# Performance work log

Measured on AMD Instinct MI355X. Metric: run time of the kernel, lower is better.

## Reference

```python
import jax, jax.numpy as jnp
import numpy as np
import math

H = 128      # hidden_channels
R = 32       # num_rbf
N = 4096     # atoms
E = 65536    # edges
CU = 4.5     # cutoff_upper (cutoff_lower = 0)
ALPHA = 5.0 / CU
MEANS = jnp.linspace(math.exp(-CU), 1.0, R, dtype=jnp.float32)
BETA = jnp.float32((2.0 / R * (1.0 - math.exp(-CU))) ** -2)
EPS = 1e-5


def _ln(x, g, b):
    mu = x.mean(-1, keepdims=True)
    var = ((x - mu) ** 2).mean(-1, keepdims=True)
    return (x - mu) * jax.lax.rsqrt(var + EPS) * g + b


def setup_inputs() -> dict:
    key = jax.random.key(0)
    ks = jax.random.split(key, 20)
    f32 = jnp.float32

    def w(i, shape):
        return jax.random.normal(ks[i], shape, f32) / np.float32(np.sqrt(shape[-1]))

    return {
        "edge_vec": jax.random.normal(ks[0], (E, 3), f32) * 1.5,
        "emb_w": w(1, (128, H)),
        "emb2_w": w(2, (H, 2 * H)), "emb2_b": jnp.zeros((H,), f32),
        "dp1_w": w(3, (H, R)), "dp1_b": jnp.zeros((H,), f32),
        "dp2_w": w(4, (H, R)), "dp2_b": jnp.zeros((H,), f32),
        "dp3_w": w(5, (H, R)), "dp3_b": jnp.zeros((H,), f32),
        "lt0_w": w(6, (H, H)), "lt1_w": w(7, (H, H)), "lt2_w": w(8, (H, H)),
        "ls0_w": w(9, (2 * H, H)), "ls0_b": jnp.zeros((2 * H,), f32),
        "ls1_w": w(10, (3 * H, 2 * H)), "ls1_b": jnp.zeros((3 * H,), f32),
        "init_g": jnp.ones((H,), f32), "init_b": jnp.zeros((H,), f32),
        "lin_w": w(11, (H, 3 * H)), "lin_b": jnp.zeros((H,), f32),
        "outn_g": jnp.ones((3 * H,), f32), "outn_b": jnp.zeros((3 * H,), f32),
        "ol1_w": w(12, (H // 2, H)), "ol1_b": jnp.zeros((H // 2,), f32),
        "ol2_w": w(13, (1, H // 2)), "ol2_b": jnp.zeros((1,), f32),
        "z": jax.random.randint(ks[14], (N,), 0, 128, dtype=jnp.int32),
        "edge_index": jax.random.randint(ks[15], (2, E), 0, N, dtype=jnp.int32),
    }


def reference(edge_vec, emb_w, emb2_w, emb2_b, dp1_w, dp1_b, dp2_w, dp2_b,
              dp3_w, dp3_b, lt0_w, lt1_w, lt2_w, ls0_w, ls0_b, ls1_w, ls1_b,
              init_g, init_b, lin_w, lin_b, outn_g, outn_b, ol1_w, ol1_b,
              ol2_w, ol2_b, z, edge_index):
    n = z.shape[0]
    src, dst = edge_index[0], edge_index[1]

    d = jnp.sqrt((edge_vec ** 2).sum(-1))                 # (E,)
    vn = edge_vec / d[:, None]                             # unit edge vectors
    cut = jnp.where(d < CU, 0.5 * (jnp.cos(jnp.pi * d / CU) + 1.0), 0.0)
    # expnorm RBF
    rbf = cut[:, None] * jnp.exp(-BETA * (jnp.exp(-ALPHA * d)[:, None] - MEANS) ** 2)  # (E,R)

    # atomic-number message Zij = emb2(cat(emb(z_i), emb(z_j)))
    zpair = jnp.concatenate([emb_w[z[src]], emb_w[z[dst]]], -1)  # (E,2H)
    zij = zpair @ emb2_w.T + emb2_b                              # (E,H)
    c = cut[:, None] * zij                                       # cutoff * Zij, (E,H)

    w1 = (rbf @ dp1_w.T + dp1_b) * c    # scalar channel weights (E,H)
    w2 = (rbf @ dp2_w.T + dp2_b) * c
    w3 = (rbf @ dp3_w.T + dp3_b) * c

    eye = jnp.eye(3, dtype=edge_vec.dtype)
    zero = jnp.zeros_like(vn[:, 0])
    skew = jnp.stack([zero, -vn[:, 2], vn[:, 1],
                      vn[:, 2], zero, -vn[:, 0],
                      -vn[:, 1], vn[:, 0], zero], 1).reshape(-1, 3, 3)  # (E,3,3)
    outer = vn[:, :, None] * vn[:, None, :]
    sym = outer - ((vn ** 2).sum(-1) / 3.0)[:, None, None] * eye        # traceless sym (E,3,3)

    seg = lambda a: jax.ops.segment_sum(a, src, num_segments=n)
    I0 = seg(w1)[:, :, None, None] * eye                                # (N,H,3,3)
    A0 = seg(w2[:, :, None, None] * skew[:, None, :, :])                # (N,H,3,3)
    S0 = seg(w3[:, :, None, None] * sym[:, None, :, :])                 # (N,H,3,3)

    tn = ((I0 + A0 + S0) ** 2).sum((-2, -1))                            # tensor_norm, (N,H)
    nrm = _ln(tn, init_g, init_b)
    h = jax.nn.silu(nrm @ ls0_w.T + ls0_b)
    scal = jax.nn.silu(h @ ls1_w.T + ls1_b).reshape(n, H, 3)            # per-channel gates

    I1 = jnp.einsum('nhxy,gh->ngxy', I0, lt0_w) * scal[..., 0][..., None, None]
    A1 = jnp.einsum('nhxy,gh->ngxy', A0, lt1_w) * scal[..., 1][..., None, None]
    S1 = jnp.einsum('nhxy,gh->ngxy', S0, lt2_w) * scal[..., 2][..., None, None]

    x = jnp.concatenate([(I1 ** 2).sum((-2, -1)),
                         (A1 ** 2).sum((-2, -1)),
                         (S1 ** 2).sum((-2, -1))], -1)                  # (N,3H)
    x = _ln(x, outn_g, outn_b)
    s1 = x @ lin_w.T + lin_b
    s2 = jax.nn.silu(s1) @ ol1_w.T + ol1_b
    s3 = jax.nn.silu(s2) @ ol2_w.T + ol2_b                              # per-atom energy (N,1)
    return s3
```

## Files before the change

kernel.cpp:

```cpp
#include <hip/hip_runtime.h>
#include <math.h>

#define NH_TOT 524288
#define N_ATOM 4096
#define N_EDGE 65536

typedef __attribute__((ext_vector_type(8))) short bf16x8;
typedef __attribute__((ext_vector_type(4))) float f32x4;

__device__ __forceinline__ unsigned short f2bf(float f) {
    unsigned u = __builtin_bit_cast(unsigned, f);
    unsigned r = (u + 0x7fffu + ((u >> 16) & 1u)) >> 16;
    return (unsigned short)r;
}
__device__ __forceinline__ float silu(float v) { return v / (1.0f + expf(-v)); }

#define WB_LS1 32768
#define WB_LT0 131072
#define WB_LT1 147456
#define WB_LT2 163840
#define WB_DP  180224

__global__ __launch_bounds__(256) void k_setup(
    const float* __restrict__ emb_w, const float* __restrict__ emb2_w,
    const int* __restrict__ ei,
    const float* __restrict__ ls0_w, const float* __restrict__ ls1_w,
    const float* __restrict__ lt0_w, const float* __restrict__ lt1_w,
    const float* __restrict__ lt2_w,
    const float* __restrict__ dp1_w, const float* __restrict__ dp2_w,
    const float* __restrict__ dp3_w,
    float* __restrict__ U1, float* __restrict__ U2,
    int* __restrict__ cnt, unsigned short* __restrict__ wb) {
    const int bx = blockIdx.x, tid = threadIdx.x;
    if (bx < 64) {
        __shared__ float se[2][128];
        const int t = bx * 2 + (tid >> 7), h = tid & 127, half = tid >> 7;
        se[half][h] = emb_w[t * 128 + h];
        __syncthreads();
        float u1 = 0.f, u2 = 0.f;
        const float* row = emb2_w + h * 256;
#pragma unroll 8
        for (int k = 0; k < 128; k++) {
            u1 += se[half][k] * row[k];
            u2 += se[half][k] * row[128 + k];
        }
        U1[t * 128 + h] = u1;
        U2[t * 128 + h] = u2;
    } else if (bx < 320) {
        const int e = (bx - 64) * 256 + tid;
        atomicAdd(&cnt[ei[e]], 1);
    } else {
        const int base = (bx - 320) * 1024 + tid * 4;
        const float* src;
        int off;
        if (base < 32768)       { src = ls0_w; off = 0; }
        else if (base < 131072) { src = ls1_w; off = 32768; }
        else if (base < 147456) { src = lt0_w; off = 131072; }
        else if (base < 163840) { src = lt1_w; off = 147456; }
        else if (base < 180224) { src = lt2_w; off = 163840; }
        else if (base < 184320) { src = dp1_w; off = 180224; }
        else if (base < 188416) { src = dp2_w; off = 184320; }
        else                    { src = dp3_w; off = 188416; }
        const float4 v = *(const float4*)(src + (base - off));
        unsigned short* o = wb + base;
        o[0] = f2bf(v.x); o[1] = f2bf(v.y); o[2] = f2bf(v.z); o[3] = f2bf(v.w);
    }
}

__global__ __launch_bounds__(256) void k_scan(const int* __restrict__ cnt, int* __restrict__ off) {
    __shared__ int s[256];
    const int t = threadIdx.x;
    int loc[16];
    int run = 0;
#pragma unroll
    for (int i = 0; i < 16; i++) { run += cnt[t * 16 + i]; loc[i] = run; }
    s[t] = run;
    __syncthreads();
    for (int d = 1; d < 256; d <<= 1) {
        const int add = (t >= d) ? s[t - d] : 0;
        __syncthreads();
        s[t] += add;
        __syncthreads();
    }
    const int base = s[t] - run;
    if (t == 0) off[0] = 0;
#pragma unroll
    for (int i = 0; i < 16; i++) off[t * 16 + i + 1] = base + loc[i];
}

__global__ __launch_bounds__(256) void k_edge(
    const float* __restrict__ edge_vec, const int* __restrict__ ei,
    const int* __restrict__ z, const int* __restrict__ off,
    int* __restrict__ cursor,
    unsigned short* __restrict__ rbf_bf, float4* __restrict__ geom,
    int* __restrict__ u2off) {
    const int e = blockIdx.x * 256 + threadIdx.x;
    const int src = ei[e];
    const int pos = off[src] + atomicAdd(&cursor[src], 1);

    const float evx = edge_vec[3 * e + 0];
    const float evy = edge_vec[3 * e + 1];
    const float evz = edge_vec[3 * e + 2];
    const float d = sqrtf(evx * evx + evy * evy + evz * evz);
    const float inv = 1.0f / d;
    const float cut = (d < 4.5f) ? 0.5f * (cosf(0.6981317007977318f * d) + 1.0f) : 0.0f;
    geom[pos] = make_float4(evx * inv, evy * inv, evz * inv, cut);
    u2off[pos] = z[ei[N_EDGE + e]] << 7;

    const float expd = expf(-1.1111111111111112f * d);
    const float m0 = 0.011108996538242306f;
    const float dm = (1.0f - m0) * (1.0f / 31.0f);
    const float tb = 0.0625f * (1.0f - m0);
    const float beta = 1.0f / (tb * tb);
    unsigned int rb[16];
#pragma unroll
    for (int r = 0; r < 16; r++) {
        const float df0 = expd - (m0 + (float)(2 * r) * dm);
        const float df1 = expd - (m0 + (float)(2 * r + 1) * dm);
        const unsigned lo = f2bf(cut * expf(-beta * df0 * df0));
        const unsigned hi = f2bf(cut * expf(-beta * df1 * df1));
        rb[r] = lo | (hi << 16);
    }
    uint4* dst = (uint4*)(rbf_bf + (size_t)pos * 32);
#pragma unroll
    for (int j = 0; j < 4; j++)
        dst[j] = make_uint4(rb[4 * j], rb[4 * j + 1], rb[4 * j + 2], rb[4 * j + 3]);
}

__global__ __launch_bounds__(256) void k_node(
    const int* __restrict__ z, const int* __restrict__ off,
    const unsigned short* __restrict__ rbf_bf, const float4* __restrict__ geom,
    const int* __restrict__ u2off,
    const float* __restrict__ U1, const float* __restrict__ U2,
    const float* __restrict__ emb2_b,
    const float* __restrict__ dp1_b, const float* __restrict__ dp2_b,
    const float* __restrict__ dp3_b,
    const unsigned short* __restrict__ wb,
    const float* __restrict__ init_g, const float* __restrict__ init_b,
    unsigned short* __restrict__ acc_bf, unsigned short* __restrict__ nrm_bf) {
    const int n = blockIdx.x, tid = threadIdx.x;
    const int wave = tid >> 6, lane = tid & 63, lm = lane & 15, lq = lane >> 4;
    const int beg = off[n];
    const int En = off[n + 1] - beg;
    const int zoff = z[n] << 7;

    const unsigned short* dpw = wb + WB_DP;
    bf16x8 bfr[3][2];
    float u1c[2], bhc[2], bk1[2], bk2[2], bk3[2];
    int cols[2];
#pragma unroll
    for (int t = 0; t < 2; t++) {
        const int col = wave * 32 + t * 16 + lm;
        cols[t] = col;
        u1c[t] = U1[zoff + col];
        bhc[t] = emb2_b[col];
        bk1[t] = dp1_b[col]; bk2[t] = dp2_b[col]; bk3[t] = dp3_b[col];
#pragma unroll
        for (int k = 0; k < 3; k++)
            bfr[k][t] = *(const bf16x8*)(dpw + k * 4096 + col * 32 + lq * 8);
    }

    float part[10][2];
#pragma unroll
    for (int p = 0; p < 10; p++) { part[p][0] = 0.f; part[p][1] = 0.f; }

    for (int mi = 0; mi < En; mi += 16) {
        const int arow = beg + min(mi + lm, En - 1);
        const bf16x8 af = *(const bf16x8*)(rbf_bf + (size_t)arow * 32 + lq * 8);
        f32x4 c[3][2];
#pragma unroll
        for (int k = 0; k < 3; k++)
#pragma unroll
            for (int t = 0; t < 2; t++)
                c[k][t] = __builtin_amdgcn_mfma_f32_16x16x32_bf16(
                    af, bfr[k][t], (f32x4){0.f, 0.f, 0.f, 0.f}, 0, 0, 0);
#pragma unroll
        for (int r = 0; r < 4; r++) {
            const int er = mi + lq * 4 + r;
            const bool valid = er < En;
            const int p = beg + (valid ? er : 0);
            const float4 g = geom[p];
            const int u2o = u2off[p];
#pragma unroll
            for (int t = 0; t < 2; t++) {
                const float u2v = U2[u2o + cols[t]];
                const float cc = valid ? g.w * (u1c[t] + u2v + bhc[t]) : 0.f;
                const float w1 = (c[0][t][r] + bk1[t]) * cc;
                const float w2 = (c[1][t][r] + bk2[t]) * cc;
                const float w3 = (c[2][t][r] + bk3[t]) * cc;
                part[0][t] += w1;
                part[1][t] += w2 * g.x; part[2][t] += w2 * g.y; part[3][t] += w2 * g.z;
                const float tx = w3 * g.x, ty = w3 * g.y;
                part[4][t] += tx * g.x; part[5][t] += tx * g.y; part[6][t] += tx * g.z;
                part[7][t] += ty * g.y; part[8][t] += ty * g.z; part[9][t] += w3 * g.z * g.z;
            }
        }
    }

    __shared__ float sP[10][128];
    __shared__ float red[128];

#pragma unroll
    for (int p = 0; p < 10; p++)
#pragma unroll
        for (int t = 0; t < 2; t++) {
            float v = part[p][t];
            v += __shfl_xor(v, 16, 64);
            v += __shfl_xor(v, 32, 64);
            if (lq == 0) {
                sP[p][cols[t]] = v;
                acc_bf[(size_t)p * NH_TOT + n * 128 + cols[t]] = f2bf(v);
            }
        }
    __syncthreads();

    float tn = 0.f, dv = 0.f;
    if (tid < 128) {
        const int h = tid;
        const float aI = sP[0][h];
        const float axv = sP[1][h], ayv = sP[2][h], azv = sP[3][h];
        const float mxx = sP[4][h], mxy = sP[5][h], mxz = sP[6][h];
        const float myy = sP[7][h], myz = sP[8][h], mzz = sP[9][h];
        const float tr3 = (mxx + myy + mzz) * (1.0f / 3.0f);
        const float t00 = aI + mxx - tr3;
        const float t11 = aI + myy - tr3;
        const float t22 = aI + mzz - tr3;
        tn = t00 * t00 + t11 * t11 + t22 * t22 +
             2.0f * (mxy * mxy + azv * azv + mxz * mxz + ayv * ayv + myz * myz + axv * axv);
        red[tid] = tn;
    }
    __syncthreads();
    for (int s = 64; s > 0; s >>= 1) { if (tid < s) red[tid] += red[tid + s]; __syncthreads(); }
    const float mu = red[0] * (1.0f / 128.0f);
    __syncthreads();
    if (tid < 128) { dv = tn - mu; red[tid] = dv * dv; }
    __syncthreads();
    for (int s = 64; s > 0; s >>= 1) { if (tid < s) red[tid] += red[tid + s]; __syncthreads(); }
    const float var = red[0] * (1.0f / 128.0f);
    if (tid < 128)
        nrm_bf[n * 128 + tid] = f2bf(dv * rsqrtf(var + 1e-5f) * init_g[tid] + init_b[tid]);
}

__global__ __launch_bounds__(256) void k_megatail(
    const unsigned short* __restrict__ nrm_bf, const unsigned short* __restrict__ acc_bf,
    const unsigned short* __restrict__ wb,
    const float* __restrict__ ls0_b, const float* __restrict__ ls1_b,
    const float* __restrict__ outn_g, const float* __restrict__ outn_b,
    const float* __restrict__ lin_w, const float* __restrict__ lin_b,
    const float* __restrict__ ol1_w, const float* __restrict__ ol1_b,
    const float* __restrict__ ol2_w, const float* __restrict__ ol2_b,
    float* __restrict__ out) {
    const int tid = threadIdx.x, wave = tid >> 6, lane = tid & 63;
    const int lm = lane & 15, lq = lane >> 4;
    const int n0 = blockIdx.x * 8;

    __shared__ unsigned short h1[16][280];
    __shared__ float scal_s[8][388];
    __shared__ float xs[8][388];
    __shared__ float ss[8][132];

    {
        f32x4 acc[4];
#pragma unroll
        for (int j = 0; j < 4; j++) acc[j] = (f32x4){0.f, 0.f, 0.f, 0.f};
        const int cbase = wave * 64;
#pragma unroll
        for (int kc = 0; kc < 128; kc += 32) {
            const int arow = n0 + min(lm, 7);
            const bf16x8 af = *(const bf16x8*)(nrm_bf + (size_t)arow * 128 + kc + lq * 8);
#pragma unroll
            for (int sn = 0; sn < 4; sn++) {
                const bf16x8 b = *(const bf16x8*)(wb + (size_t)(cbase + sn * 16 + lm) * 128 + kc + lq * 8);
                acc[sn] = __builtin_amdgcn_mfma_f32_16x16x32_bf16(af, b, acc[sn], 0, 0, 0);
            }
        }
#pragma unroll
        for (int sn = 0; sn < 4; sn++) {
            const int col = cbase + sn * 16 + lm;
            const float bv = ls0_b[col];
#pragma unroll
            for (int r = 0; r < 4; r++)
                h1[lq * 4 + r][col] = f2bf(silu(acc[sn][r] + bv));
        }
    }
    __syncthreads();
    {
        f32x4 acc[6];
#pragma unroll
        for (int j = 0; j < 6; j++) acc[j] = (f32x4){0.f, 0.f, 0.f, 0.f};
        const int cbase = wave * 96;
        const unsigned short* ls1p = wb + WB_LS1;
#pragma unroll 2
        for (int kc = 0; kc < 256; kc += 32) {
            const bf16x8 af = *(const bf16x8*)(&h1[lm][kc + lq * 8]);
#pragma unroll
            for (int sn = 0; sn < 6; sn++) {
                const bf16x8 b = *(const bf16x8*)(ls1p + (size_t)(cbase + sn * 16 + lm) * 256 + kc + lq * 8);
                acc[sn] = __builtin_amdgcn_mfma_f32_16x16x32_bf16(af, b, acc[sn], 0, 0, 0);
            }
        }
#pragma unroll
        for (int sn = 0; sn < 6; sn++) {
            const int col = cbase + sn * 16 + lm;
            const float bv = ls1_b[col];
#pragma unroll
            for (int r = 0; r < 4; r++) {
                const int node = lq * 4 + r;
                if (node < 8) scal_s[node][col] = silu(acc[sn][r] + bv);
            }
        }
    }
    __syncthreads();

    f32x4 e0[2], e1[2], e2[2], trv[2];
#pragma unroll
    for (int sn = 0; sn < 2; sn++) {
        e0[sn] = (f32x4){0.f, 0.f, 0.f, 0.f};
        e1[sn] = (f32x4){0.f, 0.f, 0.f, 0.f};
        e2[sn] = (f32x4){0.f, 0.f, 0.f, 0.f};
        trv[sn] = (f32x4){0.f, 0.f, 0.f, 0.f};
    }
#pragma unroll
    for (int p = 0; p < 10; p++) {
        const unsigned short* A = acc_bf + (size_t)p * NH_TOT;
        const unsigned short* B = wb + (p == 0 ? WB_LT0 : (p < 4 ? WB_LT1 : WB_LT2));
        f32x4 c[2];
        c[0] = (f32x4){0.f, 0.f, 0.f, 0.f};
        c[1] = (f32x4){0.f, 0.f, 0.f, 0.f};
#pragma unroll
        for (int kc = 0; kc < 128; kc += 32) {
            const int arow = n0 + min(lm, 7);
            const bf16x8 af = *(const bf16x8*)(A + (size_t)arow * 128 + kc + lq * 8);
#pragma unroll
            for (int sn = 0; sn < 2; sn++) {
                const bf16x8 b = *(const bf16x8*)(B + (size_t)(wave * 32 + sn * 16 + lm) * 128 + kc + lq * 8);
                c[sn] = __builtin_amdgcn_mfma_f32_16x16x32_bf16(af, b, c[sn], 0, 0, 0);
            }
        }
#pragma unroll
        for (int sn = 0; sn < 2; sn++) {
            if (p == 0)      e0[sn] += c[sn] * c[sn];
            else if (p < 4)  e1[sn] += c[sn] * c[sn];
            else if (p == 4 || p == 7 || p == 9) { e2[sn] += c[sn] * c[sn]; trv[sn] += c[sn]; }
            else             e2[sn] += 2.0f * c[sn] * c[sn];
        }
    }

    if (lq < 2) {
#pragma unroll
        for (int sn = 0; sn < 2; sn++) {
            const int g = wave * 32 + sn * 16 + lm;
#pragma unroll
            for (int r = 0; r < 4; r++) {
                const int node = lq * 4 + r;
                const float s0 = scal_s[node][3 * g + 0];
                const float s1 = scal_s[node][3 * g + 1];
                const float s2 = scal_s[node][3 * g + 2];
                const float a0 = 3.0f * e0[sn][r] * s0 * s0;
                const float a1 = 2.0f * e1[sn][r] * s1 * s1;
                const float tr = trv[sn][r];
                const float a2 = (e2[sn][r] - tr * tr * (1.0f / 3.0f)) * s2 * s2;
                xs[node][g] = a0;
                xs[node][128 + g] = a1;
                xs[node][256 + g] = a2;
            }
        }
    }
    __syncthreads();

#pragma unroll
    for (int i = 0; i < 2; i++) {
        const int node = wave * 2 + i;
        float v[6];
        float s = 0.f;
#pragma unroll
        for (int j = 0; j < 6; j++) { v[j] = xs[node][lane + 64 * j]; s += v[j]; }
#pragma unroll
        for (int o = 1; o < 64; o <<= 1) s += __shfl_xor(s, o, 64);
        const float mu = s * (1.0f / 384.0f);
        float q = 0.f;
#pragma unroll
        for (int j = 0; j < 6; j++) { v[j] -= mu; q += v[j] * v[j]; }
#pragma unroll
        for (int o = 1; o < 64; o <<= 1) q += __shfl_xor(q, o, 64);
        const float rs = rsqrtf(q * (1.0f / 384.0f) + 1e-5f);
#pragma unroll
        for (int j = 0; j < 6; j++) {
            const int col = lane + 64 * j;
            xs[node][col] = v[j] * rs * outn_g[col] + outn_b[col];
        }
    }
    __syncthreads();

    {
        const int j = tid & 127, half = tid >> 7;
        float a4[4];
        const float lb = lin_b[j];
#pragma unroll
        for (int i = 0; i < 4; i++) a4[i] = lb;
        const float4* wr = (const float4*)(lin_w + j * 384);
#pragma unroll 2
        for (int k4 = 0; k4 < 96; k4++) {
            const float4 w4 = wr[k4];
#pragma unroll
            for (int i = 0; i < 4; i++) {
                const float4 xv = *(const float4*)&xs[half * 4 + i][k4 * 4];
                a4[i] += w4.x * xv.x + w4.y * xv.y + w4.z * xv.z + w4.w * xv.w;
            }
        }
#pragma unroll
        for (int i = 0; i < 4; i++) ss[half * 4 + i][j] = silu(a4[i]);
    }
    __syncthreads();

    {
        const int o = tid & 63, q = tid >> 6;
        float a2v[2];
        const float ob = ol1_b[o];
        a2v[0] = ob; a2v[1] = ob;
        const float4* o4 = (const float4*)(ol1_w + o * 128);
#pragma unroll 4
        for (int k4 = 0; k4 < 32; k4++) {
            const float4 w4 = o4[k4];
#pragma unroll
            for (int i = 0; i < 2; i++) {
                const float4 sv = *(const float4*)&ss[q * 2 + i][k4 * 4];
                a2v[i] += w4.x * sv.x + w4.y * sv.y + w4.z * sv.z + w4.w * sv.w;
            }
        }
        const float w2 = ol2_w[o];
#pragma unroll
        for (int i = 0; i < 2; i++) {
            float v = silu(a2v[i]) * w2;
            for (int s = 32; s > 0; s >>= 1) v += __shfl_down(v, s, 64);
            if (o == 0) out[n0 + q * 2 + i] = v + ol2_b[0];
        }
    }
}

extern "C" void kernel_launch(void* const* d_in, const int* in_sizes, int n_in,
                              void* d_out, int out_size, void* d_ws, size_t ws_size,
                              hipStream_t stream) {
    (void)in_sizes; (void)n_in; (void)out_size; (void)ws_size;
    const float* edge_vec = (const float*)d_in[0];
    const float* emb_w   = (const float*)d_in[1];
    const float* emb2_w  = (const float*)d_in[2];
    const float* emb2_b  = (const float*)d_in[3];
    const float* dp1_w   = (const float*)d_in[4];
    const float* dp1_b   = (const float*)d_in[5];
    const float* dp2_w   = (const float*)d_in[6];
    const float* dp2_b   = (const float*)d_in[7];
    const float* dp3_w   = (const float*)d_in[8];
    const float* dp3_b   = (const float*)d_in[9];
    const float* lt0_w   = (const float*)d_in[10];
    const float* lt1_w   = (const float*)d_in[11];
    const float* lt2_w   = (const float*)d_in[12];
    const float* ls0_w   = (const float*)d_in[13];
    const float* ls0_b   = (const float*)d_in[14];
    const float* ls1_w   = (const float*)d_in[15];
    const float* ls1_b   = (const float*)d_in[16];
    const float* init_g  = (const float*)d_in[17];
    const float* init_b  = (const float*)d_in[18];
    const float* lin_w   = (const float*)d_in[19];
    const float* lin_b   = (const float*)d_in[20];
    const float* outn_g  = (const float*)d_in[21];
    const float* outn_b  = (const float*)d_in[22];
    const float* ol1_w   = (const float*)d_in[23];
    const float* ol1_b   = (const float*)d_in[24];
    const float* ol2_w   = (const float*)d_in[25];
    const float* ol2_b   = (const float*)d_in[26];
    const int* z  = (const int*)d_in[27];
    const int* ei = (const int*)d_in[28];
    float* out = (float*)d_out;

    char* w = (char*)d_ws;
    int*            cnt    = (int*)(w);
    int*            cursor = (int*)(w + 16384);
    int*            off    = (int*)(w + 32768);
    unsigned short* wb     = (unsigned short*)(w + 49408);
    float*          U1     = (float*)(w + 434432);
    float*          U2     = (float*)(w + 499968);
    int*            u2off  = (int*)(w + 565504);
    float4*         geom   = (float4*)(w + 827648);
    unsigned short* rbf_bf = (unsigned short*)(w + 1876224);
    unsigned short* nrm_bf = (unsigned short*)(w + 6070528);
    unsigned short* acc_bf = (unsigned short*)(w + 7119104);

    hipMemsetAsync(w, 0, 32768, stream);
    k_setup<<<dim3(508), dim3(256), 0, stream>>>(emb_w, emb2_w, ei,
                                                 ls0_w, ls1_w, lt0_w, lt1_w, lt2_w,
                                                 dp1_w, dp2_w, dp3_w,
                                                 U1, U2, cnt, wb);
    k_scan<<<dim3(1), dim3(256), 0, stream>>>(cnt, off);
    k_edge<<<dim3(256), dim3(256), 0, stream>>>(edge_vec, ei, z, off, cursor,
                                                rbf_bf, geom, u2off);
    k_node<<<dim3(4096), dim3(256), 0, stream>>>(z, off, rbf_bf, geom, u2off, U1, U2,
                                                 emb2_b, dp1_b, dp2_b, dp3_b, wb,
                                                 init_g, init_b, acc_bf, nrm_bf);
    k_megatail<<<dim3(512), dim3(256), 0, stream>>>(nrm_bf, acc_bf, wb, ls0_b, ls1_b,
                                                    outn_g, outn_b, lin_w, lin_b,
                                                    ol1_w, ol1_b, ol2_w, ol2_b, out);
}
```

Before: 245.8 us.

## Split tail kernel in two, halve nodes per block, use shuffle reductions

The fused tail kernel becomes two kernels. The first handles 4 nodes per block (was 8), doing the gate MLP, tensor mixing and output LayerNorm, and writes the normalized features to a global buffer. The second runs the final linear layers on 4 nodes per block. The k_node LayerNorm reduction now uses wave shuffles in place of a shared-memory tree with many barriers. This doubles the grid size to raise occupancy and parallelism, at the cost of an extra launch and a global round trip for the 4096x384 feature buffer, and it doubles weight reloads per node since each block now covers fewer nodes.

After: 305.9 us. +24.4%, slower.

```diff
diff --git a/kernel.cpp b/kernel.cpp
--- a/kernel.cpp
+++ b/kernel.cpp
@@ -198,7 +198,7 @@
     }
 
     __shared__ float sP[10][128];
-    __shared__ float red[128];
+    __shared__ float red2[4];
 
 #pragma unroll
     for (int p = 0; p < 10; p++)
@@ -214,7 +214,7 @@
         }
     __syncthreads();
 
-    float tn = 0.f, dv = 0.f;
+    float tn = 0.f;
     if (tid < 128) {
         const int h = tid;
         const float aI = sP[0][h];
@@ -227,37 +227,36 @@
         const float t22 = aI + mzz - tr3;
         tn = t00 * t00 + t11 * t11 + t22 * t22 +
              2.0f * (mxy * mxy + azv * azv + mxz * mxz + ayv * ayv + myz * myz + axv * axv);
-        red[tid] = tn;
-    }
-    __syncthreads();
-    for (int s = 64; s > 0; s >>= 1) { if (tid < s) red[tid] += red[tid + s]; __syncthreads(); }
-    const float mu = red[0] * (1.0f / 128.0f);
-    __syncthreads();
-    if (tid < 128) { dv = tn - mu; red[tid] = dv * dv; }
-    __syncthreads();
-    for (int s = 64; s > 0; s >>= 1) { if (tid < s) red[tid] += red[tid + s]; __syncthreads(); }
-    const float var = red[0] * (1.0f / 128.0f);
+    }
+    float s = tn;
+#pragma unroll
+    for (int o = 1; o < 64; o <<= 1) s += __shfl_xor(s, o, 64);
+    if (tid < 128 && lane == 0) red2[wave] = s;
+    __syncthreads();
+    const float mu = (red2[0] + red2[1]) * (1.0f / 128.0f);
+    const float dv = tn - mu;
+    float q = (tid < 128) ? dv * dv : 0.f;
+#pragma unroll
+    for (int o = 1; o < 64; o <<= 1) q += __shfl_xor(q, o, 64);
+    if (tid < 128 && lane == 0) red2[2 + wave] = q;
+    __syncthreads();
+    const float var = (red2[2] + red2[3]) * (1.0f / 128.0f);
     if (tid < 128)
         nrm_bf[n * 128 + tid] = f2bf(dv * rsqrtf(var + 1e-5f) * init_g[tid] + init_b[tid]);
 }
 
-__global__ __launch_bounds__(256) void k_megatail(
+__global__ __launch_bounds__(256) void k_gmix(
     const unsigned short* __restrict__ nrm_bf, const unsigned short* __restrict__ acc_bf,
     const unsigned short* __restrict__ wb,
     const float* __restrict__ ls0_b, const float* __restrict__ ls1_b,
     const float* __restrict__ outn_g, const float* __restrict__ outn_b,
-    const float* __restrict__ lin_w, const float* __restrict__ lin_b,
-    const float* __restrict__ ol1_w, const float* __restrict__ ol1_b,
-    const float* __restrict__ ol2_w, const float* __restrict__ ol2_b,
-    float* __restrict__ out) {
+    float* __restrict__ xs_g) {
     const int tid = threadIdx.x, wave = tid >> 6, lane = tid & 63;
     const int lm = lane & 15, lq = lane >> 4;
-    const int n0 = blockIdx.x * 8;
+    const int n0 = blockIdx.x * 4;
 
     __shared__ unsigned short h1[16][280];
-    __shared__ float scal_s[8][388];
-    __shared__ float xs[8][388];
-    __shared__ float ss[8][132];
+    __shared__ float scal_s[4][392];
 
     {
         f32x4 acc[4];
@@ -266,7 +265,7 @@
         const int cbase = wave * 64;
 #pragma unroll
         for (int kc = 0; kc < 128; kc += 32) {
-            const int arow = n0 + min(lm, 7);
+            const int arow = n0 + min(lm, 3);
             const bf16x8 af = *(const bf16x8*)(nrm_bf + (size_t)arow * 128 + kc + lq * 8);
 #pragma unroll
             for (int sn = 0; sn < 4; sn++) {
@@ -306,7 +305,7 @@
 #pragma unroll
             for (int r = 0; r < 4; r++) {
                 const int node = lq * 4 + r;
-                if (node < 8) scal_s[node][col] = silu(acc[sn][r] + bv);
+                if (node < 4) scal_s[node][col] = silu(acc[sn][r] + bv);
             }
         }
     }
@@ -329,7 +328,7 @@
         c[1] = (f32x4){0.f, 0.f, 0.f, 0.f};
 #pragma unroll
         for (int kc = 0; kc < 128; kc += 32) {
-            const int arow = n0 + min(lm, 7);
+            const int arow = n0 + min(lm, 3);
             const bf16x8 af = *(const bf16x8*)(A + (size_t)arow * 128 + kc + lq * 8);
 #pragma unroll
             for (int sn = 0; sn < 2; sn++) {
@@ -346,95 +345,112 @@
         }
     }
 
-    if (lq < 2) {
+    float xv[2][4][3];
+    if (lq == 0) {
 #pragma unroll
         for (int sn = 0; sn < 2; sn++) {
             const int g = wave * 32 + sn * 16 + lm;
 #pragma unroll
             for (int r = 0; r < 4; r++) {
-                const int node = lq * 4 + r;
-                const float s0 = scal_s[node][3 * g + 0];
-                const float s1 = scal_s[node][3 * g + 1];
-                const float s2 = scal_s[node][3 * g + 2];
-                const float a0 = 3.0f * e0[sn][r] * s0 * s0;
-                const float a1 = 2.0f * e1[sn][r] * s1 * s1;
+                const float s0 = scal_s[r][3 * g + 0];
+                const float s1 = scal_s[r][3 * g + 1];
+                const float s2 = scal_s[r][3 * g + 2];
+                xv[sn][r][0] = 3.0f * e0[sn][r] * s0 * s0;
+                xv[sn][r][1] = 2.0f * e1[sn][r] * s1 * s1;
                 const float tr = trv[sn][r];
-                const float a2 = (e2[sn][r] - tr * tr * (1.0f / 3.0f)) * s2 * s2;
-                xs[node][g] = a0;
-                xs[node][128 + g] = a1;
-                xs[node][256 + g] = a2;
-            }
-        }
-    }
-    __syncthreads();
-
-#pragma unroll
-    for (int i = 0; i < 2; i++) {
-        const int node = wave * 2 + i;
+                xv[sn][r][2] = (e2[sn][r] - tr * tr * (1.0f / 3.0f)) * s2 * s2;
+            }
+        }
+    }
+    __syncthreads();
+    if (lq == 0) {
+#pragma unroll
+        for (int sn = 0; sn < 2; sn++) {
+            const int g = wave * 32 + sn * 16 + lm;
+#pragma unroll
+            for (int r = 0; r < 4; r++) {
+                scal_s[r][g]       = xv[sn][r][0];
+                scal_s[r][128 + g] = xv[sn][r][1];
+                scal_s[r][256 + g] = xv[sn][r][2];
+            }
+        }
+    }
+    __syncthreads();
+
+    {
+        const int node = wave;
         float v[6];
         float s = 0.f;
 #pragma unroll
-        for (int j = 0; j < 6; j++) { v[j] = xs[node][lane + 64 * j]; s += v[j]; }
+        for (int j = 0; j < 6; j++) { v[j] = scal_s[node][lane + 64 * j]; s += v[j]; }
 #pragma unroll
         for (int o = 1; o < 64; o <<= 1) s += __shfl_xor(s, o, 64);
         const float mu = s * (1.0f / 384.0f);
-        float q = 0.f;
-#pragma unroll
-        for (int j = 0; j < 6; j++) { v[j] -= mu; q += v[j] * v[j]; }
-#pragma unroll
-        for (int o = 1; o < 64; o <<= 1) q += __shfl_xor(q, o, 64);
-        const float rs = rsqrtf(q * (1.0f / 384.0f) + 1e-5f);
+        float qv = 0.f;
+#pragma unroll
+        for (int j = 0; j < 6; j++) { v[j] -= mu; qv += v[j] * v[j]; }
+#pragma unroll
+        for (int o = 1; o < 64; o <<= 1) qv += __shfl_xor(qv, o, 64);
+        const float rs = rsqrtf(qv * (1.0f / 384.0f) + 1e-5f);
 #pragma unroll
         for (int j = 0; j < 6; j++) {
             const int col = lane + 64 * j;
-            xs[node][col] = v[j] * rs * outn_g[col] + outn_b[col];
-        }
+            xs_g[(size_t)(n0 + node) * 384 + col] = v[j] * rs * outn_g[col] + outn_b[col];
+        }
+    }
+}
+
+__global__ __launch_bounds__(256) void k_tail2(
+    const float* __restrict__ xs_g,
+    const float* __restrict__ lin_w, const float* __restrict__ lin_b,
+    const float* __restrict__ ol1_w, const float* __restrict__ ol1_b,
+    const float* __restrict__ ol2_w, const float* __restrict__ ol2_b,
+    float* __restrict__ out) {
+    const int tid = threadIdx.x;
+    const int n0 = blockIdx.x * 4;
+    __shared__ float xs_s[4][392];
+    __shared__ float ss[4][132];
+
+#pragma unroll
+    for (int i = 0; i < 6; i++) {
+        const int idx = tid + i * 256;
+        xs_s[idx / 384][idx % 384] = xs_g[(size_t)n0 * 384 + idx];
     }
     __syncthreads();
 
     {
         const int j = tid & 127, half = tid >> 7;
-        float a4[4];
+        float a2[2];
         const float lb = lin_b[j];
-#pragma unroll
-        for (int i = 0; i < 4; i++) a4[i] = lb;
+        a2[0] = lb; a2[1] = lb;
         const float4* wr = (const float4*)(lin_w + j * 384);
 #pragma unroll 2
         for (int k4 = 0; k4 < 96; k4++) {
             const float4 w4 = wr[k4];
 #pragma unroll
-            for (int i = 0; i < 4; i++) {
-                const float4 xv = *(const float4*)&xs[half * 4 + i][k4 * 4];
-                a4[i] += w4.x * xv.x + w4.y * xv.y + w4.z * xv.z + w4.w * xv.w;
-            }
-        }
-#pragma unroll
-        for (int i = 0; i < 4; i++) ss[half * 4 + i][j] = silu(a4[i]);
+            for (int i = 0; i < 2; i++) {
+                const float4 xv = *(const float4*)&xs_s[half * 2 + i][k4 * 4];
+                a2[i] += w4.x * xv.x + w4.y * xv.y + w4.z * xv.z + w4.w * xv.w;
+            }
+        }
+#pragma unroll
+        for (int i = 0; i < 2; i++) ss[half * 2 + i][j] = silu(a2[i]);
     }
     __syncthreads();
 
     {
         const int o = tid & 63, q = tid >> 6;
-        float a2v[2];
-        const float ob = ol1_b[o];
-        a2v[0] = ob; a2v[1] = ob;
+        float a = ol1_b[o];
         const float4* o4 = (const float4*)(ol1_w + o * 128);
 #pragma unroll 4
         for (int k4 = 0; k4 < 32; k4++) {
             const float4 w4 = o4[k4];
-#pragma unroll
-            for (int i = 0; i < 2; i++) {
-                const float4 sv = *(const float4*)&ss[q * 2 + i][k4 * 4];
-                a2v[i] += w4.x * sv.x + w4.y * sv.y + w4.z * sv.z + w4.w * sv.w;
-            }
-        }
-        const float w2 = ol2_w[o];
-#pragma unroll
-        for (int i = 0; i < 2; i++) {
-            float v = silu(a2v[i]) * w2;
-            for (int s = 32; s > 0; s >>= 1) v += __shfl_down(v, s, 64);
-            if (o == 0) out[n0 + q * 2 + i] = v + ol2_b[0];
-        }
+            const float4 sv = *(const float4*)&ss[q][k4 * 4];
+            a += w4.x * sv.x + w4.y * sv.y + w4.z * sv.z + w4.w * sv.w;
+        }
+        float v = silu(a) * ol2_w[o];
+        for (int s = 32; s > 0; s >>= 1) v += __shfl_down(v, s, 64);
+        if (o == 0) out[n0 + q] = v + ol2_b[0];
     }
 }
 
@@ -485,6 +501,7 @@
     unsigned short* rbf_bf = (unsigned short*)(w + 1876224);
     unsigned short* nrm_bf = (unsigned short*)(w + 6070528);
     unsigned short* acc_bf = (unsigned short*)(w + 7119104);
+    float*          xs_g   = (float*)(w + 22036736);
 
     hipMemsetAsync(w, 0, 32768, stream);
     k_setup<<<dim3(508), dim3(256), 0, stream>>>(emb_w, emb2_w, ei,
@@ -497,7 +514,8 @@
     k_node<<<dim3(4096), dim3(256), 0, stream>>>(z, off, rbf_bf, geom, u2off, U1, U2,
                                                  emb2_b, dp1_b, dp2_b, dp3_b, wb,
                                                  init_g, init_b, acc_bf, nrm_bf);
-    k_megatail<<<dim3(512), dim3(256), 0, stream>>>(nrm_bf, acc_bf, wb, ls0_b, ls1_b,
-                                                    outn_g, outn_b, lin_w, lin_b,
-                                                    ol1_w, ol1_b, ol2_w, ol2_b, out);
-}
+    k_gmix<<<dim3(1024), dim3(256), 0, stream>>>(nrm_bf, acc_bf, wb, ls0_b, ls1_b,
+                                                 outn_g, outn_b, xs_g);
+    k_tail2<<<dim3(1024), dim3(256), 0, stream>>>(xs_g, lin_w, lin_b,
+                                                  ol1_w, ol1_b, ol2_w, ol2_b, out);
+}
```

## Process eight atoms per k_node block with shuffle-based layernorm reductions

Applied to the files above, without the earlier changes.

k_node now launches 512 blocks that each loop over eight atoms, in place of one block per atom. The per-channel weight fragments and biases are loaded once per block and reused across the eight atoms. The tensor-norm layernorm now uses wave shuffles and a small shared array instead of the shared-memory tree reduction with many barriers. Fast intrinsics (__expf, __cosf) replace expf/cosf in the edge kernel and silu, and the xs shared array in k_megatail is padded. The cost is fewer blocks to spread the irregular per-atom edge counts across CUs, with some risk of load imbalance and tail effects.

Result: no change. 246.5 us (+0.2%).

```diff
diff --git a/kernel.cpp b/kernel.cpp
--- a/kernel.cpp
+++ b/kernel.cpp
@@ -13,7 +13,7 @@
     unsigned r = (u + 0x7fffu + ((u >> 16) & 1u)) >> 16;
     return (unsigned short)r;
 }
-__device__ __forceinline__ float silu(float v) { return v / (1.0f + expf(-v)); }
+__device__ __forceinline__ float silu(float v) { return v / (1.0f + __expf(-v)); }
 
 #define WB_LS1 32768
 #define WB_LT0 131072
@@ -103,11 +103,11 @@
     const float evz = edge_vec[3 * e + 2];
     const float d = sqrtf(evx * evx + evy * evy + evz * evz);
     const float inv = 1.0f / d;
-    const float cut = (d < 4.5f) ? 0.5f * (cosf(0.6981317007977318f * d) + 1.0f) : 0.0f;
+    const float cut = (d < 4.5f) ? 0.5f * (__cosf(0.6981317007977318f * d) + 1.0f) : 0.0f;
     geom[pos] = make_float4(evx * inv, evy * inv, evz * inv, cut);
     u2off[pos] = z[ei[N_EDGE + e]] << 7;
 
-    const float expd = expf(-1.1111111111111112f * d);
+    const float expd = __expf(-1.1111111111111112f * d);
     const float m0 = 0.011108996538242306f;
     const float dm = (1.0f - m0) * (1.0f / 31.0f);
     const float tb = 0.0625f * (1.0f - m0);
@@ -117,8 +117,8 @@
     for (int r = 0; r < 16; r++) {
         const float df0 = expd - (m0 + (float)(2 * r) * dm);
         const float df1 = expd - (m0 + (float)(2 * r + 1) * dm);
-        const unsigned lo = f2bf(cut * expf(-beta * df0 * df0));
-        const unsigned hi = f2bf(cut * expf(-beta * df1 * df1));
+        const unsigned lo = f2bf(cut * __expf(-beta * df0 * df0));
+        const unsigned hi = f2bf(cut * __expf(-beta * df1 * df1));
         rb[r] = lo | (hi << 16);
     }
     uint4* dst = (uint4*)(rbf_bf + (size_t)pos * 32);
@@ -138,21 +138,18 @@
     const unsigned short* __restrict__ wb,
     const float* __restrict__ init_g, const float* __restrict__ init_b,
     unsigned short* __restrict__ acc_bf, unsigned short* __restrict__ nrm_bf) {
-    const int n = blockIdx.x, tid = threadIdx.x;
+    const int tid = threadIdx.x;
     const int wave = tid >> 6, lane = tid & 63, lm = lane & 15, lq = lane >> 4;
-    const int beg = off[n];
-    const int En = off[n + 1] - beg;
-    const int zoff = z[n] << 7;
+    const int nb = blockIdx.x * 8;
 
     const unsigned short* dpw = wb + WB_DP;
     bf16x8 bfr[3][2];
-    float u1c[2], bhc[2], bk1[2], bk2[2], bk3[2];
+    float bhc[2], bk1[2], bk2[2], bk3[2];
     int cols[2];
 #pragma unroll
     for (int t = 0; t < 2; t++) {
         const int col = wave * 32 + t * 16 + lm;
         cols[t] = col;
-        u1c[t] = U1[zoff + col];
         bhc[t] = emb2_b[col];
         bk1[t] = dp1_b[col]; bk2[t] = dp2_b[col]; bk3[t] = dp3_b[col];
 #pragma unroll
@@ -160,85 +157,127 @@
             bfr[k][t] = *(const bf16x8*)(dpw + k * 4096 + col * 32 + lq * 8);
     }
 
-    float part[10][2];
-#pragma unroll
-    for (int p = 0; p < 10; p++) { part[p][0] = 0.f; part[p][1] = 0.f; }
-
-    for (int mi = 0; mi < En; mi += 16) {
-        const int arow = beg + min(mi + lm, En - 1);
-        const bf16x8 af = *(const bf16x8*)(rbf_bf + (size_t)arow * 32 + lq * 8);
-        f32x4 c[3][2];
-#pragma unroll
-        for (int k = 0; k < 3; k++)
-#pragma unroll
-            for (int t = 0; t < 2; t++)
-                c[k][t] = __builtin_amdgcn_mfma_f32_16x16x32_bf16(
-                    af, bfr[k][t], (f32x4){0.f, 0.f, 0.f, 0.f}, 0, 0, 0);
-#pragma unroll
-        for (int r = 0; r < 4; r++) {
-            const int er = mi + lq * 4 + r;
-            const bool valid = er < En;
-            const int p = beg + (valid ? er : 0);
-            const float4 g = geom[p];
-            const int u2o = u2off[p];
+    __shared__ float redS[8][4];
+    __shared__ float redQ[8][4];
+
+    float tnA[8], tnB[8];
+
+    for (int nn = 0; nn < 8; nn++) {
+        const int n = nb + nn;
+        const int beg = off[n];
+        const int En = off[n + 1] - beg;
+        const int zoff = z[n] << 7;
+        const float u1c0 = U1[zoff + cols[0]];
+        const float u1c1 = U1[zoff + cols[1]];
+
+        float part[10][2];
+#pragma unroll
+        for (int p = 0; p < 10; p++) { part[p][0] = 0.f; part[p][1] = 0.f; }
+
+        for (int mi = 0; mi < En; mi += 16) {
+            const int arow = beg + min(mi + lm, En - 1);
+            const bf16x8 af = *(const bf16x8*)(rbf_bf + (size_t)arow * 32 + lq * 8);
+            f32x4 c[3][2];
+#pragma unroll
+            for (int k = 0; k < 3; k++)
+#pragma unroll
+                for (int t = 0; t < 2; t++)
+                    c[k][t] = __builtin_amdgcn_mfma_f32_16x16x32_bf16(
+                        af, bfr[k][t], (f32x4){0.f, 0.f, 0.f, 0.f}, 0, 0, 0);
+#pragma unroll
+            for (int r = 0; r < 4; r++) {
+                const int er = mi + lq * 4 + r;
+                const bool valid = er < En;
+                const int p = beg + (valid ? er : 0);
+                const float4 g = geom[p];
+                const int u2o = u2off[p];
+#pragma unroll
+                for (int t = 0; t < 2; t++) {
+                    const float u2v = U2[u2o + cols[t]];
+                    const float u1h = (t == 0) ? u1c0 : u1c1;
+                    const float cc = valid ? g.w * (u1h + u2v + bhc[t]) : 0.f;
+                    const float w1 = (c[0][t][r] + bk1[t]) * cc;
+                    const float w2 = (c[1][t][r] + bk2[t]) * cc;
+                    const float w3 = (c[2][t][r] + bk3[t]) * cc;
+                    part[0][t] += w1;
+                    part[1][t] += w2 * g.x; part[2][t] += w2 * g.y; part[3][t] += w2 * g.z;
+                    const float tx = w3 * g.x, ty = w3 * g.y;
+                    part[4][t] += tx * g.x; part[5][t] += tx * g.y; part[6][t] += tx * g.z;
+                    part[7][t] += ty * g.y; part[8][t] += ty * g.z; part[9][t] += w3 * g.z * g.z;
+                }
+            }
+        }
+
+#pragma unroll
+        for (int p = 0; p < 10; p++)
 #pragma unroll
             for (int t = 0; t < 2; t++) {
-                const float u2v = U2[u2o + cols[t]];
-                const float cc = valid ? g.w * (u1c[t] + u2v + bhc[t]) : 0.f;
-                const float w1 = (c[0][t][r] + bk1[t]) * cc;
-                const float w2 = (c[1][t][r] + bk2[t]) * cc;
-                const float w3 = (c[2][t][r] + bk3[t]) * cc;
-                part[0][t] += w1;
-                part[1][t] += w2 * g.x; part[2][t] += w2 * g.y; part[3][t] += w2 * g.z;
-                const float tx = w3 * g.x, ty = w3 * g.y;
-                part[4][t] += tx * g.x; part[5][t] += tx * g.y; part[6][t] += tx * g.z;
-                part[7][t] += ty * g.y; part[8][t] += ty * g.z; part[9][t] += w3 * g.z * g.z;
-            }
-        }
-    }
-
-    __shared__ float sP[10][128];
-    __shared__ float red[128];
-
-#pragma unroll
-    for (int p = 0; p < 10; p++)
+                float v = part[p][t];
+                v += __shfl_xor(v, 16, 64);
+                v += __shfl_xor(v, 32, 64);
+                part[p][t] = v;
+            }
+        if (lq == 0) {
+#pragma unroll
+            for (int p = 0; p < 10; p++)
+#pragma unroll
+                for (int t = 0; t < 2; t++)
+                    acc_bf[(size_t)p * NH_TOT + n * 128 + cols[t]] = f2bf(part[p][t]);
+        }
+
+        float tn[2];
 #pragma unroll
         for (int t = 0; t < 2; t++) {
-            float v = part[p][t];
-            v += __shfl_xor(v, 16, 64);
-            v += __shfl_xor(v, 32, 64);
-            if (lq == 0) {
-                sP[p][cols[t]] = v;
-                acc_bf[(size_t)p * NH_TOT + n * 128 + cols[t]] = f2bf(v);
-            }
-        }
-    __syncthreads();
-
-    float tn = 0.f, dv = 0.f;
-    if (tid < 128) {
-        const int h = tid;
-        const float aI = sP[0][h];
-        const float axv = sP[1][h], ayv = sP[2][h], azv = sP[3][h];
-        const float mxx = sP[4][h], mxy = sP[5][h], mxz = sP[6][h];
-        const float myy = sP[7][h], myz = sP[8][h], mzz = sP[9][h];
-        const float tr3 = (mxx + myy + mzz) * (1.0f / 3.0f);
-        const float t00 = aI + mxx - tr3;
-        const float t11 = aI + myy - tr3;
-        const float t22 = aI + mzz - tr3;
-        tn = t00 * t00 + t11 * t11 + t22 * t22 +
-             2.0f * (mxy * mxy + azv * azv + mxz * mxz + ayv * ayv + myz * myz + axv * axv);
-        red[tid] = tn;
-    }
-    __syncthreads();
-    for (int s = 64; s > 0; s >>= 1) { if (tid < s) red[tid] += red[tid + s]; __syncthreads(); }
-    const float mu = red[0] * (1.0f / 128.0f);
-    __syncthreads();
-    if (tid < 128) { dv = tn - mu; red[tid] = dv * dv; }
-    __syncthreads();
-    for (int s = 64; s > 0; s >>= 1) { if (tid < s) red[tid] += red[tid + s]; __syncthreads(); }
-    const float var = red[0] * (1.0f / 128.0f);
-    if (tid < 128)
-        nrm_bf[n * 128 + tid] = f2bf(dv * rsqrtf(var + 1e-5f) * init_g[tid] + init_b[tid]);
+            const float aI = part[0][t];
+            const float axv = part[1][t], ayv = part[2][t], azv = part[3][t];
+            const float mxx = part[4][t], mxy = part[5][t], mxz = part[6][t];
+            const float myy = part[7][t], myz = part[8][t], mzz = part[9][t];
+            const float tr3 = (mxx + myy + mzz) * (1.0f / 3.0f);
+            const float t00 = aI + mxx - tr3;
+            const float t11 = aI + myy - tr3;
+            const float t22 = aI + mzz - tr3;
+            tn[t] = t00 * t00 + t11 * t11 + t22 * t22 +
+                    2.0f * (mxy * mxy + azv * azv + mxz * mxz + ayv * ayv + myz * myz + axv * axv);
+        }
+        tnA[nn] = tn[0];
+        tnB[nn] = tn[1];
+
+        float s = (lq == 0) ? (tn[0] + tn[1]) : 0.f;
+        s += __shfl_xor(s, 1, 64);
+        s += __shfl_xor(s, 2, 64);
+        s += __shfl_xor(s, 4, 64);
+        s += __shfl_xor(s, 8, 64);
+        if (lane == 0) redS[nn][wave] = s;
+    }
+    __syncthreads();
+
+    float dvA[8], dvB[8];
+#pragma unroll
+    for (int nn = 0; nn < 8; nn++) {
+        const float mu = (redS[nn][0] + redS[nn][1] + redS[nn][2] + redS[nn][3]) * (1.0f / 128.0f);
+        dvA[nn] = tnA[nn] - mu;
+        dvB[nn] = tnB[nn] - mu;
+        float q = (lq == 0) ? (dvA[nn] * dvA[nn] + dvB[nn] * dvB[nn]) : 0.f;
+        q += __shfl_xor(q, 1, 64);
+        q += __shfl_xor(q, 2, 64);
+        q += __shfl_xor(q, 4, 64);
+        q += __shfl_xor(q, 8, 64);
+        if (lane == 0) redQ[nn][wave] = q;
+    }
+    __syncthreads();
+
+    if (lq == 0) {
+        const float g0 = init_g[cols[0]], g1 = init_g[cols[1]];
+        const float b0 = init_b[cols[0]], b1 = init_b[cols[1]];
+#pragma unroll
+        for (int nn = 0; nn < 8; nn++) {
+            const float var = (redQ[nn][0] + redQ[nn][1] + redQ[nn][2] + redQ[nn][3]) * (1.0f / 128.0f);
+            const float rs = rsqrtf(var + 1e-5f);
+            const int n = nb + nn;
+            nrm_bf[n * 128 + cols[0]] = f2bf(dvA[nn] * rs * g0 + b0);
+            nrm_bf[n * 128 + cols[1]] = f2bf(dvB[nn] * rs * g1 + b1);
+        }
+    }
 }
 
 __global__ __launch_bounds__(256) void k_megatail(
@@ -256,7 +295,7 @@
 
     __shared__ unsigned short h1[16][280];
     __shared__ float scal_s[8][388];
-    __shared__ float xs[8][388];
+    __shared__ float xs[8][392];
     __shared__ float ss[8][132];
 
     {
@@ -356,13 +395,10 @@
                 const float s0 = scal_s[node][3 * g + 0];
                 const float s1 = scal_s[node][3 * g + 1];
                 const float s2 = scal_s[node][3 * g + 2];
-                const float a0 = 3.0f * e0[sn][r] * s0 * s0;
-                const float a1 = 2.0f * e1[sn][r] * s1 * s1;
+                xs[node][g]       = 3.0f * e0[sn][r] * s0 * s0;
+                xs[node][128 + g] = 2.0f * e1[sn][r] * s1 * s1;
                 const float tr = trv[sn][r];
-                const float a2 = (e2[sn][r] - tr * tr * (1.0f / 3.0f)) * s2 * s2;
-                xs[node][g] = a0;
-                xs[node][128 + g] = a1;
-                xs[node][256 + g] = a2;
+                xs[node][256 + g] = (e2[sn][r] - tr * tr * (1.0f / 3.0f)) * s2 * s2;
             }
         }
     }
@@ -494,9 +530,9 @@
     k_scan<<<dim3(1), dim3(256), 0, stream>>>(cnt, off);
     k_edge<<<dim3(256), dim3(256), 0, stream>>>(edge_vec, ei, z, off, cursor,
                                                 rbf_bf, geom, u2off);
-    k_node<<<dim3(4096), dim3(256), 0, stream>>>(z, off, rbf_bf, geom, u2off, U1, U2,
-                                                 emb2_b, dp1_b, dp2_b, dp3_b, wb,
-                                                 init_g, init_b, acc_bf, nrm_bf);
+    k_node<<<dim3(512), dim3(256), 0, stream>>>(z, off, rbf_bf, geom, u2off, U1, U2,
+                                                emb2_b, dp1_b, dp2_b, dp3_b, wb,
+                                                init_g, init_b, acc_bf, nrm_bf);
     k_megatail<<<dim3(512), dim3(256), 0, stream>>>(nrm_bf, acc_bf, wb, ls0_b, ls1_b,
                                                     outn_g, outn_b, lin_w, lin_b,
                                                     ol1_w, ol1_b, ol2_w, ol2_b, out);
```
